# Optimization experiments

Measured on AMD Instinct MI355X. Metric: run time of the kernel, lower is better.

Reference implementation:

```python
import jax, jax.numpy as jnp
import numpy as np

SIZE = 5
B = 262144  # batch of 5x5 boards
EPS = 1e-12  # torch F.normalize clamp


def setup_inputs() -> dict:
    key = jax.random.key(0)
    ks = jax.random.split(key, 8)
    x = jax.random.normal(ks[0], (B, SIZE, SIZE), jnp.float32)
    keep = jax.random.bernoulli(ks[1], 0.5, (B, SIZE, SIZE))
    x = jnp.where(keep, x, 0.0)
    s1 = 1.0 / np.sqrt(SIZE)
    s2 = 1.0 / np.sqrt(120.0)
    s3 = 1.0 / np.sqrt(84.0)
    W1 = jax.random.normal(ks[2], (120, SIZE), jnp.float32) * s1
    b1 = jax.random.normal(ks[3], (120,), jnp.float32) * s1
    W2 = jax.random.normal(ks[4], (84, 120), jnp.float32) * s2
    b2 = jax.random.normal(ks[5], (84,), jnp.float32) * s2
    W3 = jax.random.normal(ks[6], (SIZE, 84), jnp.float32) * s3
    b3 = jax.random.normal(ks[7], (SIZE,), jnp.float32) * s3
    return {"x": x, "W1": W1, "b1": b1, "W2": W2, "b2": b2, "W3": W3, "b3": b3}


def reference(x, W1, b1, W2, b2, W3, b3):
    # x: [B, 5, 5]; Linear applies to last dim (nn.Linear convention W[out,in])
    y = jax.nn.relu(jnp.einsum('bsi,hi->bsh', x, W1) + b1)   # [B,5,120]
    y = jax.nn.relu(jnp.einsum('bsh,gh->bsg', y, W2) + b2)   # [B,5,84]
    y = jax.nn.relu(jnp.einsum('bsg,og->bso', y, W3) + b3)   # [B,5,5]
    # F.normalize(y): L2 normalize over dim=1 of each [5,5] board = last axis here
    norm = jnp.sqrt(jnp.sum(y * y, axis=-1, keepdims=True))
    y = y / jnp.maximum(norm, EPS)
    # vectorized replacement of the nested python masking loop
    return jnp.where(x != 0.0, 0.0, y)
```

## Files before the change

### kernel.cpp

```cpp
#include <hip/hip_runtime.h>


typedef _Float16 f16x8 __attribute__((ext_vector_type(8)));
typedef _Float16 f16x4 __attribute__((ext_vector_type(4)));
typedef __fp16   hf16x2 __attribute__((ext_vector_type(2)));
typedef float    f32x4 __attribute__((ext_vector_type(4)));

#if __has_builtin(__builtin_amdgcn_mfma_f32_16x16x16f16)
#define HAVE_K16 1
#define MFMA16(a, b, c) __builtin_amdgcn_mfma_f32_16x16x16f16((a), (b), (c), 0, 0, 0)
#elif __has_builtin(__builtin_amdgcn_mfma_f32_16x16x16_f16)
#define HAVE_K16 1
#define MFMA16(a, b, c) __builtin_amdgcn_mfma_f32_16x16x16_f16((a), (b), (c), 0, 0, 0)
#else
#define HAVE_K16 0
#endif
#define MFMA32(a, b, c) __builtin_amdgcn_mfma_f32_16x16x32_f16((a), (b), (c), 0, 0, 0)
#define FZERO ((f32x4){0.f, 0.f, 0.f, 0.f})

#if __has_builtin(__builtin_amdgcn_rsqf)
#define RSQ(x) __builtin_amdgcn_rsqf(x)
#else
#define RSQ(x) (1.0f / sqrtf(x))
#endif

#define CNT_OFF  0
#define W1A_OFF  40384
#define W2A_OFF  48576
#define W3A_OFF  73152
#define LIST_OFF 76224
#define TAU2     0.04f

__device__ __forceinline__ f16x8 pack_relu8(f32x4 d0, f32x4 d1, float zf) {
    union { f16x8 v; hf16x2 h[4]; } u;
    u.h[0] = __builtin_amdgcn_cvt_pkrtz(d0[0], d0[1]);
    u.h[1] = __builtin_amdgcn_cvt_pkrtz(d0[2], d0[3]);
    u.h[2] = __builtin_amdgcn_cvt_pkrtz(d1[0], d1[1]);
    u.h[3] = __builtin_amdgcn_cvt_pkrtz(d1[2], d1[3]);
    asm("v_pk_max_f16 %0, %0, %1" : "+v"(u.h[0]) : "v"(zf));
    asm("v_pk_max_f16 %0, %0, %1" : "+v"(u.h[1]) : "v"(zf));
    asm("v_pk_max_f16 %0, %0, %1" : "+v"(u.h[2]) : "v"(zf));
    asm("v_pk_max_f16 %0, %0, %1" : "+v"(u.h[3]) : "v"(zf));
    return u.v;
}

__global__ __launch_bounds__(256) void pack_kernel(
    const float* __restrict__ W1, const float* __restrict__ b1,
    const float* __restrict__ W2, const float* __restrict__ b2,
    const float* __restrict__ W3, const float* __restrict__ b3,
    char* __restrict__ ws)
{
    int i = blockIdx.x * 256 + threadIdx.x;
    if (i == 0) *(unsigned int*)(ws + CNT_OFF) = 0u;
    _Float16* W1a = (_Float16*)(ws + W1A_OFF);
    _Float16* W2a = (_Float16*)(ws + W2A_OFF);
    _Float16* W3a = (_Float16*)(ws + W3A_OFF);

#if HAVE_K16
    if (i < 2048) {
        int n = i >> 8, l = (i >> 2) & 63, j = i & 3;
        int feat = 16*n + (l & 15);
        int k = (l >> 4) * 4 + j;
        float v = 0.f;
        if (feat < 120) {
            if (k < 5) v = W1[feat*5 + k];
            else if (k == 5) v = b1[feat];
        } else if (feat == 120 && k == 5) v = 1.f;
        W1a[i] = (_Float16)v;
    }
#else
    if (i < 4096) {
        int n = i >> 9, l = (i >> 3) & 63, j = i & 7;
        int feat = 16*n + (l & 15);
        int k = (l >> 4) * 8 + j;
        float v = 0.f;
        if (feat < 120) {
            if (k < 5) v = W1[feat*5 + k];
            else if (k == 5) v = b1[feat];
        } else if (feat == 120 && k == 5) v = 1.f;
        W1a[i] = (_Float16)v;
    }
#endif
    if (i < 12288) {
        int b = i >> 9, l = (i >> 3) & 63, j = i & 7;
        int n2 = b >> 2, t4 = b & 3;
        int g = 16*n2 + (l & 15);
        int f = 32*t4 + 16*(j >> 2) + 4*(l >> 4) + (j & 3);
        float v = 0.f;
        if (g < 84) {
            if (f < 120) v = W2[g*120 + f];
            else if (f == 120) v = b2[g];
        } else if (g == 84 && f == 120) v = 1.f;
        W2a[i] = (_Float16)v;
    }
    if (i < 1536) {
        int t3 = i >> 9, l = (i >> 3) & 63, j = i & 7;
        int o = l & 15;
        int f = 32*t3 + 16*(j >> 2) + 4*(l >> 4) + (j & 3);
        float v = 0.f;
        if (o < 5) {
            if (f < 84) v = W3[o*84 + f];
            else if (f == 84) v = b3[o];
        }
        W3a[i] = (_Float16)v;
    }
}

__global__ __launch_bounds__(256, 2) void mfma_main(
    const float* __restrict__ x, const char* __restrict__ ws,
    float* __restrict__ out,
    unsigned int* __restrict__ cnt, unsigned int* __restrict__ list,
    unsigned int cap, int nrows, int npairs)
{
    const _Float16* W1a = (const _Float16*)(ws + W1A_OFF);
    const _Float16* W2a = (const _Float16*)(ws + W2A_OFF);
    const _Float16* W3a = (const _Float16*)(ws + W3A_OFF);

    const int tid  = threadIdx.x;
    const int w    = tid >> 6, lane = tid & 63;
    const int c    = lane & 15, q = lane >> 4;
    const float zf = 0.f;

#if HAVE_K16
    f16x4 w1f[8];
#pragma unroll
    for (int n = 0; n < 8; ++n)  w1f[n] = *(const f16x4*)(W1a + (n*64 + lane)*4);
#else
    f16x8 w1f[8];
#pragma unroll
    for (int n = 0; n < 8; ++n)  w1f[n] = *(const f16x8*)(W1a + (n*64 + lane)*8);
#endif
    f16x8 w2f[24], w3f[3];
#pragma unroll
    for (int b = 0; b < 24; ++b) w2f[b] = *(const f16x8*)(W2a + (b*64 + lane)*8);
#pragma unroll
    for (int t = 0; t < 3; ++t)  w3f[t] = *(const f16x8*)(W3a + (t*64 + lane)*8);

    const int gw = blockIdx.x * 4 + w;
    const int nw = gridDim.x * 4;

    float nxA[5] = {0.f, 0.f, 0.f, 0.f, 0.f};
    float nxB[5] = {0.f, 0.f, 0.f, 0.f, 0.f};
    if (q == 0 && gw < npairs) {
        int rA = gw * 32 + c;
        int rB = rA + 16;
        if (rA < nrows) {
            const float* xp = x + rA * 5;
            nxA[0]=xp[0]; nxA[1]=xp[1]; nxA[2]=xp[2]; nxA[3]=xp[3]; nxA[4]=xp[4];
        }
        if (rB < nrows) {
            const float* xp = x + rB * 5;
            nxB[0]=xp[0]; nxB[1]=xp[1]; nxB[2]=xp[2]; nxB[3]=xp[3]; nxB[4]=xp[4];
        }
    }

    for (int p = gw; p < npairs; p += nw) {
        const int rowA = p * 32 + c;
        const int rowB = rowA + 16;
        const bool validA = (q == 0) && (rowA < nrows);
        const bool validB = (q == 0) && (rowB < nrows);

        float xA[5], xB[5];
#pragma unroll
        for (int i = 0; i < 5; ++i) { xA[i] = nxA[i]; xB[i] = nxB[i]; }

#pragma unroll
        for (int i = 0; i < 5; ++i) { nxA[i] = 0.f; nxB[i] = 0.f; }
        {
            const int pn = p + nw;
            if (q == 0 && pn < npairs) {
                int rA = pn * 32 + c;
                int rB = rA + 16;
                if (rA < nrows) {
                    const float* xp = x + rA * 5;
                    nxA[0]=xp[0]; nxA[1]=xp[1]; nxA[2]=xp[2]; nxA[3]=xp[3]; nxA[4]=xp[4];
                }
                if (rB < nrows) {
                    const float* xp = x + rB * 5;
                    nxB[0]=xp[0]; nxB[1]=xp[1]; nxB[2]=xp[2]; nxB[3]=xp[3]; nxB[4]=xp[4];
                }
            }
        }

#if HAVE_K16
        const float x4A = __shfl(xA[4], c, 64);
        const float x4B = __shfl(xB[4], c, 64);
        f16x4 axA, axB;
        {
            union { f16x4 v; hf16x2 h[2]; } ua, ub;
            float aA0 = (q == 0) ? xA[0] : ((q == 1) ? x4A : 0.f);
            float aA1 = (q == 0) ? xA[1] : ((q == 1) ? 1.f  : 0.f);
            float aA2 = (q == 0) ? xA[2] : 0.f;
            float aA3 = (q == 0) ? xA[3] : 0.f;
            float aB0 = (q == 0) ? xB[0] : ((q == 1) ? x4B : 0.f);
            float aB1 = (q == 0) ? xB[1] : ((q == 1) ? 1.f  : 0.f);
            float aB2 = (q == 0) ? xB[2] : 0.f;
            float aB3 = (q == 0) ? xB[3] : 0.f;
            ua.h[0] = __builtin_amdgcn_cvt_pkrtz(aA0, aA1);
            ua.h[1] = __builtin_amdgcn_cvt_pkrtz(aA2, aA3);
            ub.h[0] = __builtin_amdgcn_cvt_pkrtz(aB0, aB1);
            ub.h[1] = __builtin_amdgcn_cvt_pkrtz(aB2, aB3);
            axA = ua.v; axB = ub.v;
        }
#else
        f16x8 axA, axB;
#pragma unroll
        for (int j = 0; j < 8; ++j) { axA[j] = (_Float16)0.f; axB[j] = (_Float16)0.f; }
        if (validA) {
            axA[0]=(_Float16)xA[0]; axA[1]=(_Float16)xA[1]; axA[2]=(_Float16)xA[2];
            axA[3]=(_Float16)xA[3]; axA[4]=(_Float16)xA[4]; axA[5]=(_Float16)1.f;
        }
        if (validB) {
            axB[0]=(_Float16)xB[0]; axB[1]=(_Float16)xB[1]; axB[2]=(_Float16)xB[2];
            axB[3]=(_Float16)xB[3]; axB[4]=(_Float16)xB[4]; axB[5]=(_Float16)1.f;
        }
#endif

        f16x8 pbA[4], pbB[4];
#pragma unroll
        for (int t4 = 0; t4 < 4; ++t4) {
#if HAVE_K16
            f32x4 dA0 = MFMA16(w1f[2*t4],     axA, FZERO);
            f32x4 dB0 = MFMA16(w1f[2*t4],     axB, FZERO);
            f32x4 dA1 = MFMA16(w1f[2*t4 + 1], axA, FZERO);
            f32x4 dB1 = MFMA16(w1f[2*t4 + 1], axB, FZERO);
#else
            f32x4 dA0 = MFMA32(w1f[2*t4],     axA, FZERO);
            f32x4 dB0 = MFMA32(w1f[2*t4],     axB, FZERO);
            f32x4 dA1 = MFMA32(w1f[2*t4 + 1], axA, FZERO);
            f32x4 dB1 = MFMA32(w1f[2*t4 + 1], axB, FZERO);
#endif
            pbA[t4] = pack_relu8(dA0, dA1, zf);
            pbB[t4] = pack_relu8(dB0, dB1, zf);
        }

        __builtin_amdgcn_s_setprio(1);
        f32x4 accA[6], accB[6];
#pragma unroll
        for (int n2 = 0; n2 < 6; ++n2) {
            accA[n2] = MFMA32(w2f[n2*4 + 0], pbA[0], FZERO);
            accB[n2] = MFMA32(w2f[n2*4 + 0], pbB[0], FZERO);
        }
#pragma unroll
        for (int t4 = 1; t4 < 4; ++t4)
#pragma unroll
            for (int n2 = 0; n2 < 6; ++n2) {
                accA[n2] = MFMA32(w2f[n2*4 + t4], pbA[t4], accA[n2]);
                accB[n2] = MFMA32(w2f[n2*4 + t4], pbB[t4], accB[n2]);
            }
        __builtin_amdgcn_s_setprio(0);

        f16x8 phA[3], phB[3];
#pragma unroll
        for (int t3 = 0; t3 < 3; ++t3) {
            phA[t3] = pack_relu8(accA[2*t3], accA[2*t3 + 1], zf);
            phB[t3] = pack_relu8(accB[2*t3], accB[2*t3 + 1], zf);
        }

        __builtin_amdgcn_s_setprio(1);
        f32x4 acyA = MFMA32(w3f[0], phA[0], FZERO);
        f32x4 acyB = MFMA32(w3f[0], phB[0], FZERO);
#pragma unroll
        for (int t3 = 1; t3 < 3; ++t3) {
            acyA = MFMA32(w3f[t3], phA[t3], acyA);
            acyB = MFMA32(w3f[t3], phB[t3], acyB);
        }
        __builtin_amdgcn_s_setprio(0);

        float rA0 = fmaxf(acyA[0], 0.f);
        float rB0 = fmaxf(acyB[0], 0.f);
        float y4A = __shfl(rA0, c + 16, 64);
        float y4B = __shfl(rB0, c + 16, 64);
        if (validA) {
            float y0 = rA0;
            float y1 = fmaxf(acyA[1], 0.f);
            float y2 = fmaxf(acyA[2], 0.f);
            float y3 = fmaxf(acyA[3], 0.f);
            float ss = y0*y0 + y1*y1 + y2*y2 + y3*y3 + y4A*y4A;
            float inv = RSQ(fmaxf(ss, 1e-30f));
            float* op = out + rowA * 5;
            op[0] = (xA[0] != 0.f) ? 0.f : y0 * inv;
            op[1] = (xA[1] != 0.f) ? 0.f : y1 * inv;
            op[2] = (xA[2] != 0.f) ? 0.f : y2 * inv;
            op[3] = (xA[3] != 0.f) ? 0.f : y3 * inv;
            op[4] = (xA[4] != 0.f) ? 0.f : y4A * inv;
            if (ss < TAU2) {
                unsigned int idx = atomicAdd(cnt, 1u);
                if (idx < cap) list[idx] = (unsigned int)rowA;
            }
        }
        if (validB) {
            float y0 = rB0;
            float y1 = fmaxf(acyB[1], 0.f);
            float y2 = fmaxf(acyB[2], 0.f);
            float y3 = fmaxf(acyB[3], 0.f);
            float ss = y0*y0 + y1*y1 + y2*y2 + y3*y3 + y4B*y4B;
            float inv = RSQ(fmaxf(ss, 1e-30f));
            float* op = out + rowB * 5;
            op[0] = (xB[0] != 0.f) ? 0.f : y0 * inv;
            op[1] = (xB[1] != 0.f) ? 0.f : y1 * inv;
            op[2] = (xB[2] != 0.f) ? 0.f : y2 * inv;
            op[3] = (xB[3] != 0.f) ? 0.f : y3 * inv;
            op[4] = (xB[4] != 0.f) ? 0.f : y4B * inv;
            if (ss < TAU2) {
                unsigned int idx = atomicAdd(cnt, 1u);
                if (idx < cap) list[idx] = (unsigned int)rowB;
            }
        }
    }
}

__global__ __launch_bounds__(256) void rescue_kernel(
    const float* __restrict__ x,
    const float* __restrict__ W1, const float* __restrict__ b1,
    const float* __restrict__ W2, const float* __restrict__ b2,
    const float* __restrict__ W3, const float* __restrict__ b3,
    const char* __restrict__ ws, float* __restrict__ out,
    unsigned int cap, int nrows)
{
    const unsigned int* cnt  = (const unsigned int*)(ws + CNT_OFF);
    const unsigned int* list = (const unsigned int*)(ws + LIST_OFF);
    unsigned int count = *cnt;
    if (count > cap) count = cap;

    const int lane   = threadIdx.x & 63;
    const int wid    = (blockIdx.x * 256 + threadIdx.x) >> 6;
    const int nwaves = (gridDim.x * 256) >> 6;

    const int g1 = lane;
    const bool has2 = (lane < 20);
    const int g2 = has2 ? (64 + lane) : 0;

    for (unsigned int t = wid; t < count; t += nwaves) {
        long row = (long)list[t];
        if (row < 0 || row >= (long)nrows) continue;

        const float* xr = x + row * 5;
        const float xv0 = xr[0], xv1 = xr[1], xv2 = xr[2],
                    xv3 = xr[3], xv4 = xr[4];

        float acc1 = b2[g1];
        float acc2 = has2 ? b2[g2] : 0.f;
        const float* w2r1 = W2 + (size_t)g1 * 120;
        const float* w2r2 = W2 + (size_t)g2 * 120;
        for (int h = 0; h < 120; ++h) {
            float a = b1[h];
            a = fmaf(W1[h*5 + 0], xv0, a);
            a = fmaf(W1[h*5 + 1], xv1, a);
            a = fmaf(W1[h*5 + 2], xv2, a);
            a = fmaf(W1[h*5 + 3], xv3, a);
            a = fmaf(W1[h*5 + 4], xv4, a);
            a = fmaxf(a, 0.0f);
            acc1 = fmaf(w2r1[h], a, acc1);
            acc2 = fmaf(w2r2[h], a, acc2);
        }
        float h2a = fmaxf(acc1, 0.f);
        float h2b = has2 ? fmaxf(acc2, 0.f) : 0.f;

        float y[5];
#pragma unroll
        for (int o = 0; o < 5; ++o) {
            float p = W3[o*84 + g1] * h2a;
            if (has2) p = fmaf(W3[o*84 + g2], h2b, p);
#pragma unroll
            for (int s = 1; s < 64; s <<= 1) p += __shfl_xor(p, s, 64);
            y[o] = fmaxf(p + b3[o], 0.f);
        }

        if (lane == 0) {
            float ss = y[0]*y[0];
            ss = fmaf(y[1], y[1], ss);
            ss = fmaf(y[2], y[2], ss);
            ss = fmaf(y[3], y[3], ss);
            ss = fmaf(y[4], y[4], ss);
            float inv = 1.0f / fmaxf(sqrtf(ss), 1e-12f);
            float* op = out + row * 5;
#pragma unroll
            for (int o = 0; o < 5; ++o)
                op[o] = (xr[o] != 0.f) ? 0.f : y[o] * inv;
        }
    }
}

extern "C" void kernel_launch(void* const* d_in, const int* in_sizes, int n_in,
                              void* d_out, int out_size, void* d_ws, size_t ws_size,
                              hipStream_t stream) {
    const float* x  = (const float*)d_in[0];
    const float* W1 = (const float*)d_in[1];
    const float* b1 = (const float*)d_in[2];
    const float* W2 = (const float*)d_in[3];
    const float* b2 = (const float*)d_in[4];
    const float* W3 = (const float*)d_in[5];
    const float* b3 = (const float*)d_in[6];
    float* out = (float*)d_out;
    char* ws = (char*)d_ws;

    const int nrows = in_sizes[0] / 5;
    const int ntiles = (nrows + 15) / 16;
    const int npairs = (ntiles + 1) / 2;
    unsigned int cap = (ws_size > (size_t)LIST_OFF + 4)
                       ? (unsigned int)((ws_size - LIST_OFF) / 4) : 0u;
    unsigned int* cnt  = (unsigned int*)(ws + CNT_OFF);
    unsigned int* list = (unsigned int*)(ws + LIST_OFF);

    pack_kernel<<<48, 256, 0, stream>>>(W1, b1, W2, b2, W3, b3, ws);

    mfma_main<<<512, 256, 0, stream>>>(x, ws, out, cnt, list, cap,
                                       nrows, npairs);

    rescue_kernel<<<256, 256, 0, stream>>>(x, W1, b1, W2, b2, W3, b3,
                                           ws, out, cap, nrows);
}
```

Before: 66.12 us.

## Software-pipeline layer-1 MFMAs of next pair into current iteration

```diff
diff --git a/kernel.cpp b/kernel.cpp
--- a/kernel.cpp
+++ b/kernel.cpp
@@ -6,17 +6,22 @@
 typedef __fp16   hf16x2 __attribute__((ext_vector_type(2)));
 typedef float    f32x4 __attribute__((ext_vector_type(4)));
 
+#define MFMA32(a, b, c) __builtin_amdgcn_mfma_f32_16x16x32_f16((a), (b), (c), 0, 0, 0)
+#define FZERO ((f32x4){0.f, 0.f, 0.f, 0.f})
+
 #if __has_builtin(__builtin_amdgcn_mfma_f32_16x16x16f16)
-#define HAVE_K16 1
 #define MFMA16(a, b, c) __builtin_amdgcn_mfma_f32_16x16x16f16((a), (b), (c), 0, 0, 0)
 #elif __has_builtin(__builtin_amdgcn_mfma_f32_16x16x16_f16)
-#define HAVE_K16 1
 #define MFMA16(a, b, c) __builtin_amdgcn_mfma_f32_16x16x16_f16((a), (b), (c), 0, 0, 0)
 #else
-#define HAVE_K16 0
+__device__ __forceinline__ f32x4 mfma16_fb(f16x4 a, f16x4 b, f32x4 c) {
+    f16x8 a8 = {}, b8 = {};
+#pragma unroll
+    for (int i = 0; i < 4; ++i) { a8[i] = a[i]; b8[i] = b[i]; }
+    return MFMA32(a8, b8, c);
+}
+#define MFMA16(a, b, c) mfma16_fb((a), (b), (c))
 #endif
-#define MFMA32(a, b, c) __builtin_amdgcn_mfma_f32_16x16x32_f16((a), (b), (c), 0, 0, 0)
-#define FZERO ((f32x4){0.f, 0.f, 0.f, 0.f})
 
 #if __has_builtin(__builtin_amdgcn_rsqf)
 #define RSQ(x) __builtin_amdgcn_rsqf(x)
@@ -56,7 +61,6 @@
     _Float16* W2a = (_Float16*)(ws + W2A_OFF);
     _Float16* W3a = (_Float16*)(ws + W3A_OFF);
 
-#if HAVE_K16
     if (i < 2048) {
         int n = i >> 8, l = (i >> 2) & 63, j = i & 3;
         int feat = 16*n + (l & 15);
@@ -68,19 +72,6 @@
         } else if (feat == 120 && k == 5) v = 1.f;
         W1a[i] = (_Float16)v;
     }
-#else
-    if (i < 4096) {
-        int n = i >> 9, l = (i >> 3) & 63, j = i & 7;
-        int feat = 16*n + (l & 15);
-        int k = (l >> 4) * 8 + j;
-        float v = 0.f;
-        if (feat < 120) {
-            if (k < 5) v = W1[feat*5 + k];
-            else if (k == 5) v = b1[feat];
-        } else if (feat == 120 && k == 5) v = 1.f;
-        W1a[i] = (_Float16)v;
-    }
-#endif
     if (i < 12288) {
         int b = i >> 9, l = (i >> 3) & 63, j = i & 7;
         int n2 = b >> 2, t4 = b & 3;
@@ -121,15 +112,9 @@
     const int c    = lane & 15, q = lane >> 4;
     const float zf = 0.f;
 
-#if HAVE_K16
     f16x4 w1f[8];
 #pragma unroll
     for (int n = 0; n < 8; ++n)  w1f[n] = *(const f16x4*)(W1a + (n*64 + lane)*4);
-#else
-    f16x8 w1f[8];
-#pragma unroll
-    for (int n = 0; n < 8; ++n)  w1f[n] = *(const f16x8*)(W1a + (n*64 + lane)*8);
-#endif
     f16x8 w2f[24], w3f[3];
 #pragma unroll
     for (int b = 0; b < 24; ++b) w2f[b] = *(const f16x8*)(W2a + (b*64 + lane)*8);
@@ -139,19 +124,67 @@
     const int gw = blockIdx.x * 4 + w;
     const int nw = gridDim.x * 4;
 
-    float nxA[5] = {0.f, 0.f, 0.f, 0.f, 0.f};
-    float nxB[5] = {0.f, 0.f, 0.f, 0.f, 0.f};
-    if (q == 0 && gw < npairs) {
-        int rA = gw * 32 + c;
-        int rB = rA + 16;
-        if (rA < nrows) {
-            const float* xp = x + rA * 5;
-            nxA[0]=xp[0]; nxA[1]=xp[1]; nxA[2]=xp[2]; nxA[3]=xp[3]; nxA[4]=xp[4];
-        }
-        if (rB < nrows) {
-            const float* xp = x + rB * 5;
-            nxB[0]=xp[0]; nxB[1]=xp[1]; nxB[2]=xp[2]; nxB[3]=xp[3]; nxB[4]=xp[4];
-        }
+    auto LOADX = [&](int pair, float nxA[5], float nxB[5]) {
+#pragma unroll
+        for (int i = 0; i < 5; ++i) { nxA[i] = 0.f; nxB[i] = 0.f; }
+        if (q == 0 && pair < npairs) {
+            int rA = pair * 32 + c, rB = rA + 16;
+            if (rA < nrows) {
+                const float* xp = x + rA * 5;
+                nxA[0]=xp[0]; nxA[1]=xp[1]; nxA[2]=xp[2]; nxA[3]=xp[3]; nxA[4]=xp[4];
+            }
+            if (rB < nrows) {
+                const float* xp = x + rB * 5;
+                nxB[0]=xp[0]; nxB[1]=xp[1]; nxB[2]=xp[2]; nxB[3]=xp[3]; nxB[4]=xp[4];
+            }
+        }
+    };
+    auto MAKEAX = [&](const float xA[5], const float xB[5],
+                      f16x4& axA, f16x4& axB, int& mA, int& mB) {
+        const float x4A = __shfl(xA[4], c, 64);
+        const float x4B = __shfl(xB[4], c, 64);
+        union { f16x4 v; hf16x2 h[2]; } ua, ub;
+        float aA0 = (q == 0) ? xA[0] : ((q == 1) ? x4A : 0.f);
+        float aA1 = (q == 0) ? xA[1] : ((q == 1) ? 1.f  : 0.f);
+        float aA2 = (q == 0) ? xA[2] : 0.f;
+        float aA3 = (q == 0) ? xA[3] : 0.f;
+        float aB0 = (q == 0) ? xB[0] : ((q == 1) ? x4B : 0.f);
+        float aB1 = (q == 0) ? xB[1] : ((q == 1) ? 1.f  : 0.f);
+        float aB2 = (q == 0) ? xB[2] : 0.f;
+        float aB3 = (q == 0) ? xB[3] : 0.f;
+        ua.h[0] = __builtin_amdgcn_cvt_pkrtz(aA0, aA1);
+        ua.h[1] = __builtin_amdgcn_cvt_pkrtz(aA2, aA3);
+        ub.h[0] = __builtin_amdgcn_cvt_pkrtz(aB0, aB1);
+        ub.h[1] = __builtin_amdgcn_cvt_pkrtz(aB2, aB3);
+        axA = ua.v; axB = ub.v;
+        mA = (int)(xA[0] != 0.f)       | ((int)(xA[1] != 0.f) << 1)
+           | ((int)(xA[2] != 0.f) << 2) | ((int)(xA[3] != 0.f) << 3)
+           | ((int)(xA[4] != 0.f) << 4);
+        mB = (int)(xB[0] != 0.f)       | ((int)(xB[1] != 0.f) << 1)
+           | ((int)(xB[2] != 0.f) << 2) | ((int)(xB[3] != 0.f) << 3)
+           | ((int)(xB[4] != 0.f) << 4);
+    };
+    auto L1PACK = [&](f16x4 axA, f16x4 axB, f16x8 pbA[4], f16x8 pbB[4]) {
+#pragma unroll
+        for (int t4 = 0; t4 < 4; ++t4) {
+            f32x4 dA0 = MFMA16(w1f[2*t4],     axA, FZERO);
+            f32x4 dB0 = MFMA16(w1f[2*t4],     axB, FZERO);
+            f32x4 dA1 = MFMA16(w1f[2*t4 + 1], axA, FZERO);
+            f32x4 dB1 = MFMA16(w1f[2*t4 + 1], axB, FZERO);
+            pbA[t4] = pack_relu8(dA0, dA1, zf);
+            pbB[t4] = pack_relu8(dB0, dB1, zf);
+        }
+    };
+
+    float nxA[5], nxB[5];
+    f16x8 pbA[4], pbB[4];
+    int mA = 0, mB = 0;
+    {
+        LOADX(gw, nxA, nxB);
+        f16x4 axA, axB;
+        MAKEAX(nxA, nxB, axA, axB, mA, mB);
+        L1PACK(axA, axB, pbA, pbB);
+        LOADX(gw + nw, nxA, nxB);
     }
 
     for (int p = gw; p < npairs; p += nw) {
@@ -160,80 +193,6 @@
         const bool validA = (q == 0) && (rowA < nrows);
         const bool validB = (q == 0) && (rowB < nrows);
 
-        float xA[5], xB[5];
-#pragma unroll
-        for (int i = 0; i < 5; ++i) { xA[i] = nxA[i]; xB[i] = nxB[i]; }
-
-#pragma unroll
-        for (int i = 0; i < 5; ++i) { nxA[i] = 0.f; nxB[i] = 0.f; }
-        {
-            const int pn = p + nw;
-            if (q == 0 && pn < npairs) {
-                int rA = pn * 32 + c;
-                int rB = rA + 16;
-                if (rA < nrows) {
-                    const float* xp = x + rA * 5;
-                    nxA[0]=xp[0]; nxA[1]=xp[1]; nxA[2]=xp[2]; nxA[3]=xp[3]; nxA[4]=xp[4];
-                }
-                if (rB < nrows) {
-                    const float* xp = x + rB * 5;
-                    nxB[0]=xp[0]; nxB[1]=xp[1]; nxB[2]=xp[2]; nxB[3]=xp[3]; nxB[4]=xp[4];
-                }
-            }
-        }
-
-#if HAVE_K16
-        const float x4A = __shfl(xA[4], c, 64);
-        const float x4B = __shfl(xB[4], c, 64);
-        f16x4 axA, axB;
-        {
-            union { f16x4 v; hf16x2 h[2]; } ua, ub;
-            float aA0 = (q == 0) ? xA[0] : ((q == 1) ? x4A : 0.f);
-            float aA1 = (q == 0) ? xA[1] : ((q == 1) ? 1.f  : 0.f);
-            float aA2 = (q == 0) ? xA[2] : 0.f;
-            float aA3 = (q == 0) ? xA[3] : 0.f;
-            float aB0 = (q == 0) ? xB[0] : ((q == 1) ? x4B : 0.f);
-            float aB1 = (q == 0) ? xB[1] : ((q == 1) ? 1.f  : 0.f);
-            float aB2 = (q == 0) ? xB[2] : 0.f;
-            float aB3 = (q == 0) ? xB[3] : 0.f;
-            ua.h[0] = __builtin_amdgcn_cvt_pkrtz(aA0, aA1);
-            ua.h[1] = __builtin_amdgcn_cvt_pkrtz(aA2, aA3);
-            ub.h[0] = __builtin_amdgcn_cvt_pkrtz(aB0, aB1);
-            ub.h[1] = __builtin_amdgcn_cvt_pkrtz(aB2, aB3);
-            axA = ua.v; axB = ub.v;
-        }
-#else
-        f16x8 axA, axB;
-#pragma unroll
-        for (int j = 0; j < 8; ++j) { axA[j] = (_Float16)0.f; axB[j] = (_Float16)0.f; }
-        if (validA) {
-            axA[0]=(_Float16)xA[0]; axA[1]=(_Float16)xA[1]; axA[2]=(_Float16)xA[2];
-            axA[3]=(_Float16)xA[3]; axA[4]=(_Float16)xA[4]; axA[5]=(_Float16)1.f;
-        }
-        if (validB) {
-            axB[0]=(_Float16)xB[0]; axB[1]=(_Float16)xB[1]; axB[2]=(_Float16)xB[2];
-            axB[3]=(_Float16)xB[3]; axB[4]=(_Float16)xB[4]; axB[5]=(_Float16)1.f;
-        }
-#endif
-
-        f16x8 pbA[4], pbB[4];
-#pragma unroll
-        for (int t4 = 0; t4 < 4; ++t4) {
-#if HAVE_K16
-            f32x4 dA0 = MFMA16(w1f[2*t4],     axA, FZERO);
-            f32x4 dB0 = MFMA16(w1f[2*t4],     axB, FZERO);
-            f32x4 dA1 = MFMA16(w1f[2*t4 + 1], axA, FZERO);
-            f32x4 dB1 = MFMA16(w1f[2*t4 + 1], axB, FZERO);
-#else
-            f32x4 dA0 = MFMA32(w1f[2*t4],     axA, FZERO);
-            f32x4 dB0 = MFMA32(w1f[2*t4],     axB, FZERO);
-            f32x4 dA1 = MFMA32(w1f[2*t4 + 1], axA, FZERO);
-            f32x4 dB1 = MFMA32(w1f[2*t4 + 1], axB, FZERO);
-#endif
-            pbA[t4] = pack_relu8(dA0, dA1, zf);
-            pbB[t4] = pack_relu8(dB0, dB1, zf);
-        }
-
         __builtin_amdgcn_s_setprio(1);
         f32x4 accA[6], accB[6];
 #pragma unroll
@@ -250,13 +209,16 @@
             }
         __builtin_amdgcn_s_setprio(0);
 
+        f16x4 axNA, axNB; int mNA, mNB;
+        MAKEAX(nxA, nxB, axNA, axNB, mNA, mNB);
+        LOADX(p + 2*nw, nxA, nxB);
+
         f16x8 phA[3], phB[3];
 #pragma unroll
         for (int t3 = 0; t3 < 3; ++t3) {
             phA[t3] = pack_relu8(accA[2*t3], accA[2*t3 + 1], zf);
             phB[t3] = pack_relu8(accB[2*t3], accB[2*t3 + 1], zf);
         }
-
         __builtin_amdgcn_s_setprio(1);
         f32x4 acyA = MFMA32(w3f[0], phA[0], FZERO);
         f32x4 acyB = MFMA32(w3f[0], phB[0], FZERO);
@@ -266,6 +228,9 @@
             acyB = MFMA32(w3f[t3], phB[t3], acyB);
         }
         __builtin_amdgcn_s_setprio(0);
+
+        f16x8 pbNA[4], pbNB[4];
+        L1PACK(axNA, axNB, pbNA, pbNB);
 
         float rA0 = fmaxf(acyA[0], 0.f);
         float rB0 = fmaxf(acyB[0], 0.f);
@@ -279,11 +244,11 @@
             float ss = y0*y0 + y1*y1 + y2*y2 + y3*y3 + y4A*y4A;
             float inv = RSQ(fmaxf(ss, 1e-30f));
             float* op = out + rowA * 5;
-            op[0] = (xA[0] != 0.f) ? 0.f : y0 * inv;
-            op[1] = (xA[1] != 0.f) ? 0.f : y1 * inv;
-            op[2] = (xA[2] != 0.f) ? 0.f : y2 * inv;
-            op[3] = (xA[3] != 0.f) ? 0.f : y3 * inv;
-            op[4] = (xA[4] != 0.f) ? 0.f : y4A * inv;
+            op[0] = (mA & 1)  ? 0.f : y0 * inv;
+            op[1] = (mA & 2)  ? 0.f : y1 * inv;
+            op[2] = (mA & 4)  ? 0.f : y2 * inv;
+            op[3] = (mA & 8)  ? 0.f : y3 * inv;
+            op[4] = (mA & 16) ? 0.f : y4A * inv;
             if (ss < TAU2) {
                 unsigned int idx = atomicAdd(cnt, 1u);
                 if (idx < cap) list[idx] = (unsigned int)rowA;
@@ -297,16 +262,20 @@
             float ss = y0*y0 + y1*y1 + y2*y2 + y3*y3 + y4B*y4B;
             float inv = RSQ(fmaxf(ss, 1e-30f));
             float* op = out + rowB * 5;
-            op[0] = (xB[0] != 0.f) ? 0.f : y0 * inv;
-            op[1] = (xB[1] != 0.f) ? 0.f : y1 * inv;
-            op[2] = (xB[2] != 0.f) ? 0.f : y2 * inv;
-            op[3] = (xB[3] != 0.f) ? 0.f : y3 * inv;
-            op[4] = (xB[4] != 0.f) ? 0.f : y4B * inv;
+            op[0] = (mB & 1)  ? 0.f : y0 * inv;
+            op[1] = (mB & 2)  ? 0.f : y1 * inv;
+            op[2] = (mB & 4)  ? 0.f : y2 * inv;
+            op[3] = (mB & 8)  ? 0.f : y3 * inv;
+            op[4] = (mB & 16) ? 0.f : y4B * inv;
             if (ss < TAU2) {
                 unsigned int idx = atomicAdd(cnt, 1u);
                 if (idx < cap) list[idx] = (unsigned int)rowB;
             }
         }
+
+#pragma unroll
+        for (int t = 0; t < 4; ++t) { pbA[t] = pbNA[t]; pbB[t] = pbNB[t]; }
+        mA = mNA; mB = mNB;
     }
 }
 
```

New measurement: 68.04 us. +2.9%, slower.
